# Performance work log

Measured on AMD Instinct MI355X. Metric: run time of the kernel, lower is better.

Reference implementation:

```python
import jax, jax.numpy as jnp
import numpy as np
from jax import lax

NUM_GRAPHS = 64
CODEBOOK = 64
HID = 256
DIST = 8
N_NODES = 50000
EPS = 0.1
ITERS = 20
STAB = 1e-8
CLAMP_MAX = 1e6


def setup_inputs() -> dict:
    key = jax.random.key(0)
    k1, k2, k3 = jax.random.split(key, 3)
    node_distributions = jax.random.normal(k1, (N_NODES, DIST, HID), dtype=jnp.float32)
    batch_idx = jnp.sort(jax.random.randint(k2, (N_NODES,), 0, NUM_GRAPHS)).astype(jnp.int64)
    # xavier_uniform_ on [codebook_size, hidden_dim]
    bound = float(np.sqrt(6.0 / (CODEBOOK + HID)))
    codebook = jax.random.uniform(k3, (CODEBOOK, HID), minval=-bound, maxval=bound, dtype=jnp.float32)
    return {"node_distributions": node_distributions, "batch_idx": batch_idx, "codebook": codebook}


def reference(node_distributions, batch_idx, codebook):
    # Flatten: points are node-major, so segment id per point repeats batch_idx DIST times.
    x = node_distributions.reshape(-1, HID)          # [P, HID], P = N_NODES*DIST
    seg = jnp.repeat(batch_idx, DIST)                # [P]

    # Squared-Euclidean cost matrix against codebook, clamped at 0.
    x_norm = jnp.sum(x * x, axis=1, keepdims=True)   # [P, 1]
    y_norm = jnp.sum(codebook * codebook, axis=1)    # [K]
    cost = jnp.maximum(x_norm + y_norm[None, :] - 2.0 * (x @ codebook.T), 0.0)  # [P, K]

    Kmat = jnp.exp(-cost / EPS)
    Kmat = jnp.where(jnp.isnan(Kmat) | jnp.isinf(Kmat), STAB, Kmat)

    # Per-graph marginals: a = 1/(rows in graph), b = 1/K.
    counts = jax.ops.segment_sum(jnp.ones_like(batch_idx, dtype=jnp.float32), batch_idx, num_segments=NUM_GRAPHS)  # nodes/graph
    n_rows = counts * DIST                           # flattened rows per graph
    a = 1.0 / jnp.maximum(n_rows, 1.0)[seg]          # [P] (empty graphs have no points)
    b_marg = 1.0 / CODEBOOK

    u0 = jnp.ones(x.shape[0], dtype=x.dtype)
    v0 = jnp.ones((NUM_GRAPHS, CODEBOOK), dtype=x.dtype)

    def step(carry, _):
        u, v = carry
        Kv = jnp.sum(Kmat * v[seg], axis=1)                          # [P]
        u = a / jnp.maximum(Kv, STAB)
        KTu = jax.ops.segment_sum(Kmat * u[:, None], seg, num_segments=NUM_GRAPHS)  # [B, K]
        v = b_marg / jnp.maximum(KTu, STAB)
        return (u, v), None

    (u, v), _ = lax.scan(step, (u0, v0), None, length=ITERS)

    uc = jnp.clip(u, STAB, CLAMP_MAX)
    vc = jnp.clip(v, STAB, CLAMP_MAX)

    # Column sums of transport matrix per graph: sum_p uc_p * K[p,k] * vc[b,k]
    wsum = jax.ops.segment_sum(Kmat * uc[:, None], seg, num_segments=NUM_GRAPHS) * vc  # [B, K]
    total = jnp.sum(wsum, axis=1, keepdims=True)

    normed = jnp.where(total > STAB, wsum / jnp.maximum(total, STAB), 1.0 / CODEBOOK)
    # Graphs with zero nodes are skipped in the original (stay zero).
    out = jnp.where(counts[:, None] == 0, 0.0, normed)
    return out
```

## Files before the change

kernel.cpp:

```cpp
#include <hip/hip_runtime.h>

#define NG 64
#define KK 64
#define HIDDEN 256
#define DIST 8
#define NNODES 50000
#define PTOT (NNODES*DIST)
#define EPSV 0.1f
#define NITERS 20
#define STABV 1e-8f
#define CMAXV 1e6f

#define CERT_COST 64.0f

#define OFF_AINV 0
#define OFF_COUNTS 64
#define OFF_NNZ 128
#define OFF_NSUS 129
#define OFF_MAXY 130
#define OFF_YN 192
#define OFF_SUS 256
#define OFF_ROWSEG (OFF_SUS + PTOT)
#define OFF_UC (OFF_ROWSEG + PTOT)
#define OFF_KROWS (OFF_UC + PTOT)

__global__ __launch_bounds__(256) void init_kernel(float* ws) {
  int t = threadIdx.x;
  if (t == 0) { ((int*)(ws + OFF_NNZ))[0] = 0; ((int*)(ws + OFF_NSUS))[0] = 0; }
  if (t < NG) ((int*)(ws + OFF_COUNTS))[t] = 0;
}

__global__ __launch_bounds__(256) void counts_kernel(const int* __restrict__ bidx,
                                                     float* ws) {
  __shared__ int h[NG];
  int t = threadIdx.x;
  if (t < NG) h[t] = 0;
  __syncthreads();
  int i = blockIdx.x * 256 + t;
  if (i < NNODES) atomicAdd(&h[bidx[i]], 1);
  __syncthreads();
  if (t < NG && h[t] > 0) atomicAdd(&((int*)(ws + OFF_COUNTS))[t], h[t]);
}

__global__ __launch_bounds__(64) void ainv_kernel(float* ws) {
  int g = threadIdx.x;
  int c = ((int*)(ws + OFF_COUNTS))[g];
  ws[OFF_AINV + g] = 1.0f / fmaxf((float)(c * DIST), 1.0f);
}

__global__ __launch_bounds__(64) void cbnorm_kernel(const float* __restrict__ cb,
                                                    float* ws) {
  int lane = threadIdx.x;
  const float4* cb4 = (const float4*)cb;
  float yn = 0.0f;
  for (int j = 0; j < 64; j++) {
    float4 c = cb4[lane * 64 + j];
    yn = fmaf(c.x, c.x, fmaf(c.y, c.y, fmaf(c.z, c.z, fmaf(c.w, c.w, yn))));
  }
  ws[OFF_YN + lane] = yn;
  float ymax = sqrtf(yn);
#pragma unroll
  for (int m = 1; m < 64; m <<= 1) ymax = fmaxf(ymax, __shfl_xor(ymax, m));
  if (lane == 0) ws[OFF_MAXY] = ymax;
}

__global__ __launch_bounds__(256) void norm_suspect_kernel(const float* __restrict__ x,
                                                           float* __restrict__ ws) {
  int tid = threadIdx.x;
  int wave = tid >> 6, lane = tid & 63;
  size_t pbase = (size_t)blockIdx.x * 32 + (size_t)wave * 8;
  const float4* x4 = (const float4*)x;
  float maxy = ws[OFF_MAXY];

  float4 xv[8];
#pragma unroll
  for (int i = 0; i < 8; i++) xv[i] = x4[(pbase + i) * 64 + lane];
  float s[8];
#pragma unroll
  for (int i = 0; i < 8; i++)
    s[i] = fmaf(xv[i].x, xv[i].x, fmaf(xv[i].y, xv[i].y,
           fmaf(xv[i].z, xv[i].z, xv[i].w * xv[i].w)));
#pragma unroll
  for (int m = 1; m < 64; m <<= 1) {
#pragma unroll
    for (int i = 0; i < 8; i++) s[i] += __shfl_xor(s[i], m);
  }
  float mine = 0.0f;
#pragma unroll
  for (int i = 0; i < 8; i++) if (lane == i) mine = s[i];
  if (lane < 8) {
    float r = sqrtf(mine) - maxy;
    bool safe = (mine < 1e30f) && (r > 0.0f) && (r * r > CERT_COST);
    if (!safe) {
      int slot = atomicAdd((int*)(ws + OFF_NSUS), 1);
      if (slot < PTOT) ((int*)(ws + OFF_SUS))[slot] = (int)(pbase + lane);
    }
  }
}

__global__ __launch_bounds__(256) void suspect_kernel(const float* __restrict__ x,
    const int* __restrict__ bidx, const float* __restrict__ cb,
    float* __restrict__ ws, int cap) {
  int tid = threadIdx.x;
  int wave = tid >> 6, lane = tid & 63;
  int nsus = ((int*)(ws + OFF_NSUS))[0];
  if (nsus > PTOT) nsus = PTOT;
  const int* sus = (const int*)(ws + OFF_SUS);
  const float4* x4 = (const float4*)x;
  const float4* cb4 = (const float4*)cb;
  int gw = blockIdx.x * 4 + wave, nw = gridDim.x * 4;
  for (int si = gw; si < nsus; si += nw) {
    int p = sus[si];
    float4 xv = x4[(size_t)p * 64 + lane];
    float xn = fmaf(xv.x, xv.x, fmaf(xv.y, xv.y, fmaf(xv.z, xv.z, xv.w * xv.w)));
#pragma unroll
    for (int m = 1; m < 64; m <<= 1) xn += __shfl_xor(xn, m);
    float myk = 0.0f;
    for (int k = 0; k < 64; k++) {
      float4 c = cb4[k * 64 + lane];
      float d = fmaf(xv.x, c.x, fmaf(xv.y, c.y, fmaf(xv.z, c.z, xv.w * c.w)));
#pragma unroll
      for (int m = 1; m < 64; m <<= 1) d += __shfl_xor(d, m);
      float cost = fmaxf(xn + ws[OFF_YN + k] - 2.0f * d, 0.0f);
      float km = __expf(cost * (-1.0f / EPSV));
      if (!(km <= 1.0f)) km = STABV;
      if (lane == k) myk = km;
    }
    unsigned long long nz = __ballot(myk != 0.0f);
    if (nz != 0ull) {
      int slot = 0;
      if (lane == 0) slot = atomicAdd((int*)(ws + OFF_NNZ), 1);
      slot = __shfl(slot, 0);
      if (slot < cap) {
        (ws + OFF_KROWS)[(size_t)slot * 64 + lane] = myk;
        if (lane == 0) ((int*)(ws + OFF_ROWSEG))[slot] = bidx[p >> 3];
      }
    }
  }
}

__global__ __launch_bounds__(256) void solve_kernel(float* __restrict__ ws,
                                                    float* __restrict__ out, int cap) {
  __shared__ float vsh[NG * KK];
  __shared__ float ash[NG * KK];
  __shared__ float tot[NG];
  int tid = threadIdx.x;
  int wave = tid >> 6, lane = tid & 63;
  int nnz = ((int*)(ws + OFF_NNZ))[0];
  if (nnz > cap) nnz = cap;
  const float* krows = ws + OFF_KROWS;
  const int* rowseg = (const int*)(ws + OFF_ROWSEG);
  const int* counts = (const int*)(ws + OFF_COUNTS);
  float* uc = ws + OFF_UC;

  for (int i = tid; i < NG * KK; i += 256) vsh[i] = 1.0f;
  __syncthreads();

  for (int it = 0; it < NITERS; it++) {
    for (int i = tid; i < NG * KK; i += 256) ash[i] = 0.0f;
    __syncthreads();
    for (int r = wave; r < nnz; r += 4) {
      int g = rowseg[r];
      float kw = krows[(size_t)r * 64 + lane];
      float kv = kw * vsh[(g << 6) | lane];
#pragma unroll
      for (int m = 1; m < 64; m <<= 1) kv += __shfl_xor(kv, m);
      float u = ws[OFF_AINV + g] / fmaxf(kv, STABV);
      if (it == NITERS - 1 && lane == 0) uc[r] = u;
      atomicAdd(&ash[(g << 6) | lane], kw * u);
    }
    __syncthreads();
    for (int i = tid; i < NG * KK; i += 256)
      vsh[i] = (1.0f / KK) / fmaxf(ash[i], STABV);
    __syncthreads();
  }

  for (int i = tid; i < NG * KK; i += 256) ash[i] = 0.0f;
  __syncthreads();
  for (int r = wave; r < nnz; r += 4) {
    int g = rowseg[r];
    float kw = krows[(size_t)r * 64 + lane];
    float u = fminf(fmaxf(uc[r], STABV), CMAXV);
    atomicAdd(&ash[(g << 6) | lane], kw * u);
  }
  __syncthreads();
  for (int i = tid; i < NG * KK; i += 256) {
    float vv = fminf(fmaxf(vsh[i], STABV), CMAXV);
    ash[i] = ash[i] * vv;
  }
  __syncthreads();
  if (tid < NG) {
    float s = 0.0f;
    for (int k = 0; k < KK; k++) s += ash[(tid << 6) + k];
    tot[tid] = s;
  }
  __syncthreads();
  for (int i = tid; i < NG * KK; i += 256) {
    int g = i >> 6;
    float val;
    if (counts[g] == 0) val = 0.0f;
    else if (tot[g] > STABV) val = ash[i] / fmaxf(tot[g], STABV);
    else val = 1.0f / KK;
    out[i] = val;
  }
}

extern "C" void kernel_launch(void* const* d_in, const int* in_sizes, int n_in,
                              void* d_out, int out_size, void* d_ws, size_t ws_size,
                              hipStream_t stream) {
  const float* x = (const float*)d_in[0];
  const int* bidx = (const int*)d_in[1];
  const float* cb = (const float*)d_in[2];
  float* ws = (float*)d_ws;
  float* out = (float*)d_out;

  long cap_l = ((long)(ws_size / 4) - OFF_KROWS) / 64;
  if (cap_l < 0) cap_l = 0;
  if (cap_l > PTOT) cap_l = PTOT;
  int cap = (int)cap_l;

  init_kernel<<<1, 256, 0, stream>>>(ws);
  counts_kernel<<<(NNODES + 255) / 256, 256, 0, stream>>>(bidx, ws);
  ainv_kernel<<<1, 64, 0, stream>>>(ws);
  cbnorm_kernel<<<1, 64, 0, stream>>>(cb, ws);
  norm_suspect_kernel<<<PTOT / 32, 256, 0, stream>>>(x, ws);
  suspect_kernel<<<64, 256, 0, stream>>>(x, bidx, cb, ws, cap);
  solve_kernel<<<1, 256, 0, stream>>>(ws, out, cap);
}
```

Measured before the change: 571.2 us.

## Fuse init/count/norm kernels and tighten suspect-filter threshold

Merges the counts, ainv and codebook-norm kernels into fewer launches, moving the counts histogram into the main norm-scan kernel and ainv into the solve kernel. The norm scan now uses quarter-waves per point, handling four points per load batch so that reductions need fewer shuffles. The certification threshold changes from a margin of sqrt(64) to about 3.6 plus a small slack, which marks fewer points as suspects. It also skips the Sinkhorn loop when there are no nonzero rows. A dead suspect_kernel stub is left in but never launched. The tighter threshold risks missing rows whose exp(-cost/eps) is tiny but not zero.

```diff
diff --git a/kernel.cpp b/kernel.cpp
--- a/kernel.cpp
+++ b/kernel.cpp
@@ -2,7 +2,6 @@
 
 #define NG 64
 #define KK 64
-#define HIDDEN 256
 #define DIST 8
 #define NNODES 50000
 #define PTOT (NNODES*DIST)
@@ -11,114 +10,136 @@
 #define STABV 1e-8f
 #define CMAXV 1e6f
 
-#define CERT_COST 64.0f
-
-#define OFF_AINV 0
-#define OFF_COUNTS 64
-#define OFF_NNZ 128
-#define OFF_NSUS 129
-#define OFF_MAXY 130
-#define OFF_YN 192
-#define OFF_SUS 256
+#define OFF_COUNTS 0
+#define OFF_NNZ 64
+#define OFF_NSUS 65
+#define OFF_MAXY 66
+#define OFF_YN 128
+#define OFF_SUS 192
 #define OFF_ROWSEG (OFF_SUS + PTOT)
 #define OFF_UC (OFF_ROWSEG + PTOT)
 #define OFF_KROWS (OFF_UC + PTOT)
 
-__global__ __launch_bounds__(256) void init_kernel(float* ws) {
-  int t = threadIdx.x;
-  if (t == 0) { ((int*)(ws + OFF_NNZ))[0] = 0; ((int*)(ws + OFF_NSUS))[0] = 0; }
-  if (t < NG) ((int*)(ws + OFF_COUNTS))[t] = 0;
-}
-
-__global__ __launch_bounds__(256) void counts_kernel(const int* __restrict__ bidx,
-                                                     float* ws) {
-  __shared__ int h[NG];
-  int t = threadIdx.x;
-  if (t < NG) h[t] = 0;
-  __syncthreads();
-  int i = blockIdx.x * 256 + t;
-  if (i < NNODES) atomicAdd(&h[bidx[i]], 1);
-  __syncthreads();
-  if (t < NG && h[t] > 0) atomicAdd(&((int*)(ws + OFF_COUNTS))[t], h[t]);
-}
-
-__global__ __launch_bounds__(64) void ainv_kernel(float* ws) {
-  int g = threadIdx.x;
-  int c = ((int*)(ws + OFF_COUNTS))[g];
-  ws[OFF_AINV + g] = 1.0f / fmaxf((float)(c * DIST), 1.0f);
-}
-
-__global__ __launch_bounds__(64) void cbnorm_kernel(const float* __restrict__ cb,
-                                                    float* ws) {
-  int lane = threadIdx.x;
+__device__ __forceinline__ float dot4(float4 a, float4 b) {
+  return fmaf(a.x, b.x, fmaf(a.y, b.y, fmaf(a.z, b.z, a.w * b.w)));
+}
+
+__global__ __launch_bounds__(256) void init_kernel(const float* __restrict__ cb,
+                                                   float* __restrict__ ws) {
+  __shared__ float ynsh[KK];
+  int t = threadIdx.x, w = t >> 6, l = t & 63;
+  if (t < NG) ((int*)ws)[OFF_COUNTS + t] = 0;
+  if (t == 0) { ((int*)ws)[OFF_NNZ] = 0; ((int*)ws)[OFF_NSUS] = 0; }
   const float4* cb4 = (const float4*)cb;
-  float yn = 0.0f;
-  for (int j = 0; j < 64; j++) {
-    float4 c = cb4[lane * 64 + j];
-    yn = fmaf(c.x, c.x, fmaf(c.y, c.y, fmaf(c.z, c.z, fmaf(c.w, c.w, yn))));
-  }
-  ws[OFF_YN + lane] = yn;
-  float ymax = sqrtf(yn);
-#pragma unroll
-  for (int m = 1; m < 64; m <<= 1) ymax = fmaxf(ymax, __shfl_xor(ymax, m));
-  if (lane == 0) ws[OFF_MAXY] = ymax;
-}
-
-__global__ __launch_bounds__(256) void norm_suspect_kernel(const float* __restrict__ x,
-                                                           float* __restrict__ ws) {
+#pragma unroll
+  for (int it = 0; it < 16; it++) {
+    float4 c = cb4[it * 256 + t];
+    float e = dot4(c, c);
+#pragma unroll
+    for (int m = 1; m < 64; m <<= 1) e += __shfl_xor(e, m);
+    if (l == 0) ynsh[it * 4 + w] = e;
+  }
+  __syncthreads();
+  if (t < KK) {
+    float yn = ynsh[t];
+    ws[OFF_YN + t] = yn;
+    float ym = sqrtf(yn);
+#pragma unroll
+    for (int m = 1; m < 64; m <<= 1) ym = fmaxf(ym, __shfl_xor(ym, m));
+    if (t == 0) ws[OFF_MAXY] = ym;
+  }
+}
+
+__global__ __launch_bounds__(256) void main_kernel(const float* __restrict__ x,
+    const int* __restrict__ bidx, float* __restrict__ ws) {
+  __shared__ int hist[NG];
+  int t = threadIdx.x, w = t >> 6, l = t & 63;
+  int b = blockIdx.x;
+  if (t < NG) hist[t] = 0;
+  __syncthreads();
+  if (t < 40) atomicAdd(&hist[bidx[b * 40 + t] & 63], 1);
+  __syncthreads();
+  if (t < NG && hist[t] > 0) atomicAdd(&((int*)ws)[OFF_COUNTS + t], hist[t]);
+
+  float maxy = ws[OFF_MAXY];
+  float thr = fmaf(maxy, 1.0001f, 0.01f) + 3.6f;
+  float thr2 = thr * thr;
+  const float4* x4 = (const float4*)x;
+  int q = l >> 4, r = l & 15;
+  int base = b * 320 + w * 80;
+  int* nsusp = &((int*)ws)[OFF_NSUS];
+  int* sus = &((int*)ws)[OFF_SUS];
+#pragma unroll
+  for (int o = 0; o < 5; o++) {
+    int p0 = base + o * 16;
+    float4 v0 = x4[(size_t)(p0 + q) * 64 + r];
+    float4 v1 = x4[(size_t)(p0 + 4 + q) * 64 + r];
+    float4 v2 = x4[(size_t)(p0 + 8 + q) * 64 + r];
+    float4 v3 = x4[(size_t)(p0 + 12 + q) * 64 + r];
+    float s0 = dot4(v0, v0), s1 = dot4(v1, v1), s2 = dot4(v2, v2), s3 = dot4(v3, v3);
+#pragma unroll
+    for (int m = 1; m < 16; m <<= 1) {
+      s0 += __shfl_xor(s0, m); s1 += __shfl_xor(s1, m);
+      s2 += __shfl_xor(s2, m); s3 += __shfl_xor(s3, m);
+    }
+    if (r == 0) {
+      float ss[4] = {s0, s1, s2, s3};
+#pragma unroll
+      for (int i = 0; i < 4; i++) {
+        bool safe = (ss[i] > thr2) && (ss[i] < 1e30f);
+        if (!safe) {
+          int slot = atomicAdd(nsusp, 1);
+          if (slot < PTOT) sus[slot] = p0 + 4 * i + q;
+        }
+      }
+    }
+  }
+}
+
+__global__ __launch_bounds__(256) void suspect_kernel(const float* __restrict__ x,
+    const int* __restrict__ bidx, float* __restrict__ ws, int cap) {
   int tid = threadIdx.x;
   int wave = tid >> 6, lane = tid & 63;
-  size_t pbase = (size_t)blockIdx.x * 32 + (size_t)wave * 8;
+  int nsus = ((int*)ws)[OFF_NSUS];
+  if (nsus > PTOT) nsus = PTOT;
+  const int* sus = &((int*)ws)[OFF_SUS];
   const float4* x4 = (const float4*)x;
-  float maxy = ws[OFF_MAXY];
-
-  float4 xv[8];
-#pragma unroll
-  for (int i = 0; i < 8; i++) xv[i] = x4[(pbase + i) * 64 + lane];
-  float s[8];
-#pragma unroll
-  for (int i = 0; i < 8; i++)
-    s[i] = fmaf(xv[i].x, xv[i].x, fmaf(xv[i].y, xv[i].y,
-           fmaf(xv[i].z, xv[i].z, xv[i].w * xv[i].w)));
-#pragma unroll
-  for (int m = 1; m < 64; m <<= 1) {
-#pragma unroll
-    for (int i = 0; i < 8; i++) s[i] += __shfl_xor(s[i], m);
-  }
-  float mine = 0.0f;
-#pragma unroll
-  for (int i = 0; i < 8; i++) if (lane == i) mine = s[i];
-  if (lane < 8) {
-    float r = sqrtf(mine) - maxy;
-    bool safe = (mine < 1e30f) && (r > 0.0f) && (r * r > CERT_COST);
-    if (!safe) {
-      int slot = atomicAdd((int*)(ws + OFF_NSUS), 1);
-      if (slot < PTOT) ((int*)(ws + OFF_SUS))[slot] = (int)(pbase + lane);
-    }
-  }
-}
-
-__global__ __launch_bounds__(256) void suspect_kernel(const float* __restrict__ x,
+  int gw = blockIdx.x * 4 + wave, nw = gridDim.x * 4;
+  for (int si = gw; si < nsus; si += nw) {
+    int p = sus[si];
+    float4 xv = x4[(size_t)p * 64 + lane];
+    float xn = dot4(xv, xv);
+#pragma unroll
+    for (int m = 1; m < 64; m <<= 1) xn += __shfl_xor(xn, m);
+    float myk = 0.0f;
+    for (int k = 0; k < KK; k++) {
+      k = k;
+    }
+    (void)myk; (void)xn;
+  }
+}
+
+__global__ __launch_bounds__(256) void suspect2_kernel(const float* __restrict__ x,
     const int* __restrict__ bidx, const float* __restrict__ cb,
     float* __restrict__ ws, int cap) {
   int tid = threadIdx.x;
   int wave = tid >> 6, lane = tid & 63;
-  int nsus = ((int*)(ws + OFF_NSUS))[0];
+  int nsus = ((int*)ws)[OFF_NSUS];
   if (nsus > PTOT) nsus = PTOT;
-  const int* sus = (const int*)(ws + OFF_SUS);
+  const int* sus = &((int*)ws)[OFF_SUS];
   const float4* x4 = (const float4*)x;
   const float4* cb4 = (const float4*)cb;
   int gw = blockIdx.x * 4 + wave, nw = gridDim.x * 4;
   for (int si = gw; si < nsus; si += nw) {
     int p = sus[si];
     float4 xv = x4[(size_t)p * 64 + lane];
-    float xn = fmaf(xv.x, xv.x, fmaf(xv.y, xv.y, fmaf(xv.z, xv.z, xv.w * xv.w)));
+    float xn = dot4(xv, xv);
 #pragma unroll
     for (int m = 1; m < 64; m <<= 1) xn += __shfl_xor(xn, m);
     float myk = 0.0f;
-    for (int k = 0; k < 64; k++) {
+    for (int k = 0; k < KK; k++) {
       float4 c = cb4[k * 64 + lane];
-      float d = fmaf(xv.x, c.x, fmaf(xv.y, c.y, fmaf(xv.z, c.z, xv.w * c.w)));
+      float d = dot4(xv, c);
 #pragma unroll
       for (int m = 1; m < 64; m <<= 1) d += __shfl_xor(d, m);
       float cost = fmaxf(xn + ws[OFF_YN + k] - 2.0f * d, 0.0f);
@@ -129,11 +150,11 @@
     unsigned long long nz = __ballot(myk != 0.0f);
     if (nz != 0ull) {
       int slot = 0;
-      if (lane == 0) slot = atomicAdd((int*)(ws + OFF_NNZ), 1);
+      if (lane == 0) slot = atomicAdd(&((int*)ws)[OFF_NNZ], 1);
       slot = __shfl(slot, 0);
       if (slot < cap) {
         (ws + OFF_KROWS)[(size_t)slot * 64 + lane] = myk;
-        if (lane == 0) ((int*)(ws + OFF_ROWSEG))[slot] = bidx[p >> 3];
+        if (lane == 0) ((int*)ws)[OFF_ROWSEG + slot] = bidx[p >> 3];
       }
     }
   }
@@ -144,46 +165,50 @@
   __shared__ float vsh[NG * KK];
   __shared__ float ash[NG * KK];
   __shared__ float tot[NG];
+  __shared__ float ainv[NG];
   int tid = threadIdx.x;
   int wave = tid >> 6, lane = tid & 63;
-  int nnz = ((int*)(ws + OFF_NNZ))[0];
+  int nnz = ((int*)ws)[OFF_NNZ];
   if (nnz > cap) nnz = cap;
   const float* krows = ws + OFF_KROWS;
-  const int* rowseg = (const int*)(ws + OFF_ROWSEG);
-  const int* counts = (const int*)(ws + OFF_COUNTS);
+  const int* rowseg = &((int*)ws)[OFF_ROWSEG];
+  const int* counts = &((int*)ws)[OFF_COUNTS];
   float* uc = ws + OFF_UC;
 
-  for (int i = tid; i < NG * KK; i += 256) vsh[i] = 1.0f;
-  __syncthreads();
-
-  for (int it = 0; it < NITERS; it++) {
+  if (tid < NG) ainv[tid] = 1.0f / fmaxf((float)(counts[tid] * DIST), 1.0f);
+  for (int i = tid; i < NG * KK; i += 256) { vsh[i] = 1.0f; ash[i] = 0.0f; }
+  __syncthreads();
+
+  if (nnz > 0) {
+    for (int it = 0; it < NITERS; it++) {
+      for (int i = tid; i < NG * KK; i += 256) ash[i] = 0.0f;
+      __syncthreads();
+      for (int r = wave; r < nnz; r += 4) {
+        int g = rowseg[r];
+        float kw = krows[(size_t)r * 64 + lane];
+        float kv = kw * vsh[(g << 6) | lane];
+#pragma unroll
+        for (int m = 1; m < 64; m <<= 1) kv += __shfl_xor(kv, m);
+        float u = ainv[g] / fmaxf(kv, STABV);
+        if (it == NITERS - 1 && lane == 0) uc[r] = u;
+        atomicAdd(&ash[(g << 6) | lane], kw * u);
+      }
+      __syncthreads();
+      for (int i = tid; i < NG * KK; i += 256)
+        vsh[i] = (1.0f / KK) / fmaxf(ash[i], STABV);
+      __syncthreads();
+    }
     for (int i = tid; i < NG * KK; i += 256) ash[i] = 0.0f;
     __syncthreads();
     for (int r = wave; r < nnz; r += 4) {
       int g = rowseg[r];
       float kw = krows[(size_t)r * 64 + lane];
-      float kv = kw * vsh[(g << 6) | lane];
-#pragma unroll
-      for (int m = 1; m < 64; m <<= 1) kv += __shfl_xor(kv, m);
-      float u = ws[OFF_AINV + g] / fmaxf(kv, STABV);
-      if (it == NITERS - 1 && lane == 0) uc[r] = u;
+      float u = fminf(fmaxf(uc[r], STABV), CMAXV);
       atomicAdd(&ash[(g << 6) | lane], kw * u);
     }
     __syncthreads();
-    for (int i = tid; i < NG * KK; i += 256)
-      vsh[i] = (1.0f / KK) / fmaxf(ash[i], STABV);
-    __syncthreads();
-  }
-
-  for (int i = tid; i < NG * KK; i += 256) ash[i] = 0.0f;
-  __syncthreads();
-  for (int r = wave; r < nnz; r += 4) {
-    int g = rowseg[r];
-    float kw = krows[(size_t)r * 64 + lane];
-    float u = fminf(fmaxf(uc[r], STABV), CMAXV);
-    atomicAdd(&ash[(g << 6) | lane], kw * u);
-  }
-  __syncthreads();
+  }
+
   for (int i = tid; i < NG * KK; i += 256) {
     float vv = fminf(fmaxf(vsh[i], STABV), CMAXV);
     ash[i] = ash[i] * vv;
@@ -219,11 +244,8 @@
   if (cap_l > PTOT) cap_l = PTOT;
   int cap = (int)cap_l;
 
-  init_kernel<<<1, 256, 0, stream>>>(ws);
-  counts_kernel<<<(NNODES + 255) / 256, 256, 0, stream>>>(bidx, ws);
-  ainv_kernel<<<1, 64, 0, stream>>>(ws);
-  cbnorm_kernel<<<1, 64, 0, stream>>>(cb, ws);
-  norm_suspect_kernel<<<PTOT / 32, 256, 0, stream>>>(x, ws);
-  suspect_kernel<<<64, 256, 0, stream>>>(x, bidx, cb, ws, cap);
+  init_kernel<<<1, 256, 0, stream>>>(cb, ws);
+  main_kernel<<<NNODES / 40, 256, 0, stream>>>(x, bidx, ws);
+  suspect2_kernel<<<64, 256, 0, stream>>>(x, bidx, cb, ws, cap);
   solve_kernel<<<1, 256, 0, stream>>>(ws, out, cap);
 }
```

New measurement: 479.2 us. 1.19x faster.
